# Performance work log

Hardware: AMD Instinct MI355X
Metric: run time of the kernel (lower is better)

The kernel has to match this reference:

```python
import jax, jax.numpy as jnp
import numpy as np

D = 1024   # visual_dim
N = 64     # num_phrases(1) * topN(64)
DEG = 16   # edges per subject row (incl. one guaranteed via a permutation)
E = N * DEG
T = 2      # cfg.MODEL.RELATION.VISUAL_GRAPH_PASSING_TIME


def _graph():
    rng = np.random.default_rng(0)
    perm = rng.permutation(N)
    mask = np.zeros((N, N), bool)
    for i in range(N):
        mask[i, perm[i]] = True  # permutation guarantees every column is covered
        pool = np.delete(np.arange(N), perm[i])
        mask[i, rng.choice(pool, DEG - 1, replace=False)] = True
    hdim, wdim = np.nonzero(mask)  # row-major, exactly E entries
    conn = np.full((N, N), -1, np.int32)
    conn[hdim, wdim] = np.arange(hdim.shape[0])
    edge_idx = hdim * N + wdim  # original: hdim*topN + wdim (topN == N since num_phrases == 1)
    return conn, edge_idx.astype(np.int32)


def setup_inputs():
    conn, edge_idx = _graph()
    key = jax.random.key(0)
    ks = jax.random.split(key, 16)
    p = lambda k, shp: jax.random.normal(k, shp, jnp.float32) * 0.02
    return {
        'visual_feat': jax.random.normal(ks[0], (N, D), jnp.float32),
        'rel_visual_feat': jax.random.normal(ks[1], (E, D), jnp.float32),
        'conn_map': jnp.asarray(conn),
        'topN_boxes_ids': jnp.arange(N, dtype=jnp.int32)[None, :],  # only shape is used
        'edge_idx': jnp.asarray(edge_idx),
        'W_sub': p(ks[2], (D, D)),
        'W_obj': p(ks[3], (D, D)),
        'W_r2s': p(ks[4], (D, D)),
        'W_r2o': p(ks[5], (D, D)),
        'W_joint': p(ks[6], (D, 4 * D)),
        'W_ctx': p(ks[7], (D, 3 * D)),
        'W_rel_update': p(ks[8], (D, 3 * D)),
        'W_rel_joint': p(ks[9], (D, 4 * D)),
        'W_rel_ctx': p(ks[10], (D, 2 * D)),
        'W_node': p(ks[11], (D, 2 * D)),
        'b_node': jnp.zeros((D,), jnp.float32),
        'W_factor': p(ks[12], (D, 2 * D)),
    }


def _forward(visual_feat, rel_visual_feat, conn_map, edge_idx,
             W_sub, W_obj, W_r2s, W_r2o, W_joint, W_ctx, W_rel_update,
             W_rel_joint, W_rel_ctx, W_node, b_node, W_factor):
    n, d = visual_feat.shape
    scale = jnp.asarray(d, visual_feat.dtype) ** 0.5
    connected = conn_map >= 0
    # scatter edge features into the dense [N, N, D] grid
    rel_temp = (jnp.zeros((n * n, d), visual_feat.dtype)
                .at[edge_idx].set(rel_visual_feat)
                .reshape(n, n, d))
    rel_ctx = rel_temp
    vctx = visual_feat
    for _ in range(T):
        # joint node embedding  [N, D]
        vj = jnp.concatenate([visual_feat, vctx, visual_feat * vctx, vctx - visual_feat], 1) @ W_joint.T
        # joint edge embedding  [N, N, D] (1x1 conv == per-position linear)
        rj = jnp.einsum('ijd,od->ijo',
                        jnp.concatenate([rel_temp, rel_ctx, rel_temp * rel_ctx, rel_temp - rel_ctx], 2),
                        W_rel_joint)
        # node -> edge: cat(sub_tile, obj_tile, rj) @ W_rel_update, done without tiling
        Ws, Wo, Wr = W_rel_update[:, :d], W_rel_update[:, d:2 * d], W_rel_update[:, 2 * d:]
        rel_j = (vj @ Ws.T)[:, None, :] + (vj @ Wo.T)[None, :, :] + jnp.einsum('ijd,od->ijo', rj, Wr)
        # edge -> node attention scores (elementwise product of 1x1-conv outputs, summed over channels)
        s_sbj = jnp.einsum('id,ijd->ij', vj @ W_sub.T, jnp.einsum('ijd,od->ijo', rel_j, W_r2s)) / scale
        s_obj = jnp.einsum('jd,ijd->ij', vj @ W_obj.T, jnp.einsum('ijd,od->ijo', rel_j, W_r2o)) / scale
        w_sbj = jax.nn.softmax(jnp.where(connected, s_sbj, -jnp.inf), axis=1)
        w_obj = jax.nn.softmax(jnp.where(connected, s_obj, -jnp.inf), axis=0)
        ctx = jnp.concatenate([jnp.einsum('ijd,ij->id', rel_j, w_sbj),
                               jnp.einsum('ijd,ij->jd', rel_j, w_obj)], 1)
        vctx = jnp.concatenate([vctx, ctx], 1) @ W_ctx.T
        rel_ctx = jnp.einsum('ijd,od->ijo', jnp.concatenate([rel_ctx, rel_j], 2), W_rel_ctx)
    # gather back the valid edges and produce outputs
    rel_out = jnp.concatenate([rel_visual_feat, rel_ctx.reshape(-1, d)[edge_idx]], 1) @ W_factor.T
    v_out = jnp.concatenate([visual_feat, vctx], 1) @ W_node.T + b_node
    deg = connected.sum(1) + connected.sum(0)
    v_out = jnp.where((deg == 0)[:, None], visual_feat, v_out)  # isolated nodes pass through
    return rel_out, v_out


def reference(visual_feat, rel_visual_feat, conn_map, topN_boxes_ids, edge_idx,
              W_sub, W_obj, W_r2s, W_r2o, W_joint, W_ctx, W_rel_update,
              W_rel_joint, W_rel_ctx, W_node, b_node, W_factor):
    del topN_boxes_ids  # only its shape is used in the original
    return _forward(visual_feat, rel_visual_feat, conn_map, edge_idx,
                    W_sub, W_obj, W_r2s, W_r2o, W_joint, W_ctx, W_rel_update,
                    W_rel_joint, W_rel_ctx, W_node, b_node, W_factor)
```

## Files before the change

kernel.cpp:

```cpp
#include <hip/hip_runtime.h>

static constexpr int kN = 64;
static constexpr int kD = 1024;
static constexpr int kE = 1024;
static constexpr int kT = 2;

typedef short  bf16x8 __attribute__((ext_vector_type(8)));
typedef float  f32x4  __attribute__((ext_vector_type(4)));
typedef unsigned short us8 __attribute__((ext_vector_type(8)));
typedef unsigned short us4 __attribute__((ext_vector_type(4)));

__device__ __forceinline__ unsigned short f2b(float f) {
    unsigned int u = __builtin_bit_cast(unsigned int, f);
    u += 0x7FFFu + ((u >> 16) & 1u);
    return (unsigned short)(u >> 16);
}
__device__ __forceinline__ float b2f(unsigned short u) {
    unsigned int x = ((unsigned int)u) << 16;
    return __builtin_bit_cast(float, x);
}
__device__ __forceinline__ bf16x8 cvt8(float4 a, float4 b) {
    us8 o;
    o[0] = f2b(a.x); o[1] = f2b(a.y); o[2] = f2b(a.z); o[3] = f2b(a.w);
    o[4] = f2b(b.x); o[5] = f2b(b.y); o[6] = f2b(b.z); o[7] = f2b(b.w);
    return __builtin_bit_cast(bf16x8, o);
}

struct ASrc { const unsigned short* s0; const unsigned short* s1; const unsigned short* s2;
              int mode; int ld; };

__device__ __forceinline__ bf16x8 loadA8(const ASrc& s, int row, int kg) {
    const int seg = kg >> 10, k = kg & 1023;
    const size_t ro = (size_t)row * s.ld + k;
    if (s.mode == 1) {
        const unsigned short* p = (seg == 0) ? s.s0 : (seg == 1 ? s.s1 : s.s2);
        return *(const bf16x8*)(p + ro);
    }
    const bf16x8 a = *(const bf16x8*)(s.s0 + ro);
    if (seg == 0) return a;
    const bf16x8 b = *(const bf16x8*)(s.s1 + ro);
    const us8 ua = __builtin_bit_cast(us8, a), ub = __builtin_bit_cast(us8, b);
    us8 o;
#pragma unroll
    for (int q = 0; q < 8; ++q) o[q] = f2b(b2f(ua[q]) * b2f(ub[q]));
    return __builtin_bit_cast(bf16x8, o);
}

struct GJob { ASrc a; const unsigned short* W; int ldw; void* P; int M; int K; int KS; int pbf; };
struct GJobs { GJob j[8]; int t0[9]; int nj; };

__global__ __launch_bounds__(256)
void k_gemm(GJobs G)
{
    __shared__ unsigned short lds[12288];
    const int flat = blockIdx.x;
    int ji = 0;
    while (ji + 1 < G.nj && flat >= G.t0[ji + 1]) ++ji;
    const GJob J = G.j[ji];
    const int local = flat - G.t0[ji];
    const int rowTiles = J.M >> 6;
    const int rt = local & (rowTiles - 1);
    const int rest = local / rowTiles;
    const int ct = rest & 7, z = rest >> 3;
    const int rowBase = rt * 64, colBase = ct * 128;
    const int kchunk = J.K / J.KS, kbeg = z * kchunk, kend = kbeg + kchunk;

    const int tid = threadIdx.x, lane = tid & 63, wid = tid >> 6;
    const int l15 = lane & 15, l4 = lane >> 4;
    const int sr = tid >> 3, sc8 = tid & 7;
    const int wc8 = (sc8 ^ (sr & 7)) * 8;
    const int wr = wid >> 1, wc = wid & 1;

    bf16x8 ra[2], rb[4];
    auto stage = [&](int kt) {
#pragma unroll
        for (int h = 0; h < 2; ++h)
            ra[h] = loadA8(J.a, rowBase + sr + 32 * h, kt + sc8 * 8);
#pragma unroll
        for (int h = 0; h < 4; ++h)
            rb[h] = *(const bf16x8*)(J.W + (size_t)(colBase + sr + 32 * h) * J.ldw + kt + sc8 * 8);
    };

    f32x4 acc[2][4] = {};
    stage(kbeg);
    for (int kt = kbeg; kt < kend; kt += 64) {
        __syncthreads();
#pragma unroll
        for (int h = 0; h < 2; ++h)
            *(bf16x8*)&lds[(sr + 32 * h) * 64 + wc8] = ra[h];
#pragma unroll
        for (int h = 0; h < 4; ++h)
            *(bf16x8*)&lds[4096 + (sr + 32 * h) * 64 + wc8] = rb[h];
        __syncthreads();
        if (kt + 64 < kend) stage(kt + 64);
#pragma unroll
        for (int kk = 0; kk < 2; ++kk) {
            const int c8 = kk * 4 + l4;
            bf16x8 af[2], bv[4];
#pragma unroll
            for (int m = 0; m < 2; ++m) {
                const int ar = wr * 32 + m * 16 + l15;
                af[m] = *(const bf16x8*)&lds[ar * 64 + (c8 ^ (ar & 7)) * 8];
            }
#pragma unroll
            for (int n = 0; n < 4; ++n) {
                const int br = wc * 64 + n * 16 + l15;
                bv[n] = *(const bf16x8*)&lds[4096 + br * 64 + (c8 ^ (br & 7)) * 8];
            }
#pragma unroll
            for (int m = 0; m < 2; ++m)
#pragma unroll
                for (int n = 0; n < 4; ++n)
                    acc[m][n] = __builtin_amdgcn_mfma_f32_16x16x32_bf16(af[m], bv[n], acc[m][n], 0, 0, 0);
        }
    }

    if (J.pbf) {
        __syncthreads();
#pragma unroll
        for (int m = 0; m < 2; ++m)
#pragma unroll
            for (int n = 0; n < 4; ++n)
#pragma unroll
                for (int r = 0; r < 4; ++r)
                    lds[(wr * 32 + m * 16 + l4 * 4 + r) * 132 + wc * 64 + n * 16 + l15] =
                        f2b(acc[m][n][r]);
        __syncthreads();
        unsigned short* Pb = (unsigned short*)J.P + (size_t)z * J.M * 1024;
#pragma unroll
        for (int c = tid; c < 1024; c += 256) {
            const int row = c >> 4, ch = c & 15;
            *(bf16x8*)(Pb + (size_t)(rowBase + row) * 1024 + colBase + ch * 8) =
                *(const bf16x8*)&lds[row * 132 + ch * 8];
        }
    } else {
        float* base = (float*)J.P + (size_t)z * J.M * 1024;
#pragma unroll
        for (int m = 0; m < 2; ++m) {
            const int row = rowBase + wr * 32 + m * 16 + l4 * 4;
#pragma unroll
            for (int n = 0; n < 4; ++n) {
                const int col = colBase + wc * 64 + n * 16 + l15;
#pragma unroll
                for (int r = 0; r < 4; ++r)
                    base[(size_t)(row + r) * 1024 + col] = acc[m][n][r];
            }
        }
    }
}

struct RJob { const void* P; int MO8; int KS; int pbf; float* Cf; unsigned short* Cb;
              const unsigned short* addb; const float* bias; int gather;
              const float* gP; int ostride; };
struct RJobs { RJob j[8]; int t0[9]; int nj; const int* eidx; int gKS; };

__global__ void k_reduce(RJobs R)
{
    const int flat = blockIdx.x;
    int ji = 0;
    while (ji + 1 < R.nj && flat >= R.t0[ji + 1]) ++ji;
    const RJob J = R.j[ji];
    const int i8 = (flat - R.t0[ji]) * 256 + threadIdx.x;
    if (i8 >= J.MO8) return;
    float s[8] = {0.f, 0.f, 0.f, 0.f, 0.f, 0.f, 0.f, 0.f};
    if (J.pbf) {
        const unsigned short* P = (const unsigned short*)J.P;
        for (int z = 0; z < J.KS; ++z) {
            const us8 v = *(const us8*)(P + (size_t)z * J.MO8 * 8 + (size_t)i8 * 8);
#pragma unroll
            for (int q = 0; q < 8; ++q) s[q] += b2f(v[q]);
        }
    } else {
        const float* P = (const float*)J.P;
        for (int z = 0; z < J.KS; ++z) {
            const float* p = P + (size_t)z * J.MO8 * 8 + (size_t)i8 * 8;
            const float4 v0 = *(const float4*)p;
            const float4 v1 = *(const float4*)(p + 4);
            s[0] += v0.x; s[1] += v0.y; s[2] += v0.z; s[3] += v0.w;
            s[4] += v1.x; s[5] += v1.y; s[6] += v1.z; s[7] += v1.w;
        }
    }
    if (J.addb) {
        const us8 v = *(const us8*)(J.addb + (size_t)i8 * 8);
#pragma unroll
        for (int q = 0; q < 8; ++q) s[q] += b2f(v[q]);
    }
    if (J.gather) {
        const int e = i8 >> 7, c8 = i8 & 127;
        const int idx = R.eidx[e];
        const float* as_ = J.gP + (size_t)(idx >> 6) * 1024 + c8 * 8;
        const float* ao_ = J.gP + 131072 + (size_t)(idx & 63) * 1024 + c8 * 8;
        for (int z = 0; z < R.gKS; ++z) {
#pragma unroll
            for (int q = 0; q < 8; ++q)
                s[q] += as_[(size_t)z * 65536 + q] + ao_[(size_t)z * 65536 + q];
        }
    }
    if (J.bias) {
        const int c8 = i8 & 127;
#pragma unroll
        for (int q = 0; q < 8; ++q) s[q] += J.bias[c8 * 8 + q];
    }
    if (J.Cf) {
        *(float4*)(J.Cf + (size_t)i8 * 8)     = make_float4(s[0], s[1], s[2], s[3]);
        *(float4*)(J.Cf + (size_t)i8 * 8 + 4) = make_float4(s[4], s[5], s[6], s[7]);
    }
    if (J.Cb) {
        us8 o;
#pragma unroll
        for (int q = 0; q < 8; ++q) o[q] = f2b(s[q]);
        if (J.ostride) {
            const int row = i8 >> 7, c8 = i8 & 127;
            *(us8*)(J.Cb + (size_t)row * J.ostride + c8 * 8) = o;
        } else {
            *(us8*)(J.Cb + (size_t)i8 * 8) = o;
        }
    }
}

struct ConvBatch { const float* s[7]; unsigned short* d[7]; int beg8[7]; int total8; };
__global__ void k_f2b_batch(ConvBatch cb)
{
    int i = blockIdx.x * blockDim.x + threadIdx.x;
    if (i >= cb.total8) return;
    int k = 0;
    while (k < 6 && i >= cb.beg8[k + 1]) ++k;
    const int j = i - cb.beg8[k];
    const float4 v0 = reinterpret_cast<const float4*>(cb.s[k])[2 * j];
    const float4 v1 = reinterpret_cast<const float4*>(cb.s[k])[2 * j + 1];
    const bf16x8 o = cvt8(v0, v1);
    *(bf16x8*)(cb.d[k] + (size_t)j * 8) = o;
}

struct TJ { const float* s; unsigned short* d; int ld; };
struct T7 { TJ t[7]; };
__global__ __launch_bounds__(256)
void k_transpose(T7 t7)
{
    __shared__ float tile[64][65];
    const TJ tj = t7.t[blockIdx.z];
    const int bx = blockIdx.x * 64, by = blockIdx.y * 64;
    const int c = threadIdx.x & 63, r0 = threadIdx.x >> 6;
#pragma unroll
    for (int h = 0; h < 16; ++h) {
        const int r = r0 * 16 + h;
        tile[r][c] = tj.s[(size_t)(by + r) * tj.ld + bx + c];
    }
    __syncthreads();
#pragma unroll
    for (int h = 0; h < 16; ++h) {
        const int kk = r0 * 16 + h;
        tj.d[(size_t)(bx + kk) * 1024 + by + c] = f2b(tile[c][kk]);
    }
}

__global__ __launch_bounds__(256)
void k_buildW(const float* __restrict__ Wrel, const float* __restrict__ Wjnt,
              unsigned short* __restrict__ WrtRel, unsigned short* __restrict__ WeffRel,
              unsigned short* __restrict__ UrtVj, unsigned short* __restrict__ UeffVj)
{
    const int idx = blockIdx.x * 256 + threadIdx.x;
    const int o = idx >> 8, j = (idx & 255) * 4;
    const float* W = blockIdx.z ? Wjnt : Wrel;
    const float sgn = blockIdx.z ? -1.f : 1.f;
    unsigned short* rt = blockIdx.z ? UrtVj : WrtRel;
    unsigned short* ef = blockIdx.z ? UeffVj : WeffRel;
    const float4 w1 = *(const float4*)(W + (size_t)o * 4096 + j);
    const float4 w2 = *(const float4*)(W + (size_t)o * 4096 + 1024 + j);
    const float4 w3 = *(const float4*)(W + (size_t)o * 4096 + 2048 + j);
    const float4 w4 = *(const float4*)(W + (size_t)o * 4096 + 3072 + j);
    us4 t;
    t.x = f2b(w1.x + sgn * w4.x); t.y = f2b(w1.y + sgn * w4.y);
    t.z = f2b(w1.z + sgn * w4.z); t.w = f2b(w1.w + sgn * w4.w);
    *(us4*)(rt + (size_t)o * 1024 + j) = t;
    t.x = f2b(w2.x - sgn * w4.x); t.y = f2b(w2.y - sgn * w4.y);
    t.z = f2b(w2.z - sgn * w4.z); t.w = f2b(w2.w - sgn * w4.w);
    *(us4*)(ef + (size_t)o * 2048 + j) = t;
    t.x = f2b(w3.x); t.y = f2b(w3.y); t.z = f2b(w3.z); t.w = f2b(w3.w);
    *(us4*)(ef + (size_t)o * 2048 + 1024 + j) = t;
}

__global__ __launch_bounds__(256)
void k_sctx(const float* __restrict__ relj, const float* __restrict__ qws,
            const float* __restrict__ qwo, const int* __restrict__ conn,
            unsigned short* __restrict__ ctx1b, unsigned short* __restrict__ ctx2b)
{
    const int bid = blockIdx.x, t = threadIdx.x;
    const float4* relj4 = reinterpret_cast<const float4*>(relj);
    __shared__ float sl[64];
    __shared__ int el[64];
    float4 acc = make_float4(0.f, 0.f, 0.f, 0.f);

    if (bid < 64) {
        const int i = bid;
        {
            const int g = t >> 4, l = t & 15;
            const size_t e4 = (size_t)(i * 16 + g) * 256;
            const float4* q4 = reinterpret_cast<const float4*>(qws) + (size_t)i * 256;
            float v = 0.f;
#pragma unroll
            for (int q = 0; q < 16; ++q) {
                const float4 r = relj4[e4 + l + q * 16];
                const float4 a = q4[l + q * 16];
                v += a.x * r.x + a.y * r.y + a.z * r.z + a.w * r.w;
            }
            v += __shfl_xor(v, 1, 16);
            v += __shfl_xor(v, 2, 16);
            v += __shfl_xor(v, 4, 16);
            v += __shfl_xor(v, 8, 16);
            if (l == 0) sl[g] = v * 0.03125f;
        }
        __syncthreads();
        float sv[16];
        float m = -1e30f;
#pragma unroll
        for (int q = 0; q < 16; ++q) { sv[q] = sl[q]; m = fmaxf(m, sv[q]); }
        float sum = 0.f;
#pragma unroll
        for (int q = 0; q < 16; ++q) { sv[q] = expf(sv[q] - m); sum += sv[q]; }
        const float inv = 1.f / sum;
#pragma unroll
        for (int q = 0; q < 16; ++q) {
            const float w = sv[q] * inv;
            const float4 v = relj4[(size_t)(i * 16 + q) * 256 + t];
            acc.x += w * v.x; acc.y += w * v.y; acc.z += w * v.z; acc.w += w * v.w;
        }
        us4 o; o.x = f2b(acc.x); o.y = f2b(acc.y); o.z = f2b(acc.z); o.w = f2b(acc.w);
        *(us4*)(ctx1b + (size_t)i * 1024 + t * 4) = o;
    } else {
        const int j = bid - 64;
        {
            const int i = t >> 2, sub = t & 3;
            const int e = conn[i * kN + j];
            if (sub == 0) el[i] = e;
            float v = 0.f;
            if (e >= 0) {
                const size_t e4 = (size_t)e * 256;
                const float4* q4 = reinterpret_cast<const float4*>(qwo) + (size_t)j * 256;
#pragma unroll
                for (int q = 0; q < 64; ++q) {
                    const float4 r = relj4[e4 + sub + q * 4];
                    const float4 a = q4[sub + q * 4];
                    v += a.x * r.x + a.y * r.y + a.z * r.z + a.w * r.w;
                }
            }
            v += __shfl_xor(v, 1, 4);
            v += __shfl_xor(v, 2, 4);
            if (sub == 0) sl[i] = (e >= 0) ? v * 0.03125f : -1e30f;
        }
        __syncthreads();
        float m = -1e30f;
        for (int i = 0; i < 64; ++i) m = fmaxf(m, sl[i]);
        float sum = 0.f;
        float ex[64];
        for (int i = 0; i < 64; ++i) {
            ex[i] = (el[i] >= 0) ? expf(sl[i] - m) : 0.f;
            sum += ex[i];
        }
        const float inv = 1.f / sum;
        for (int i = 0; i < 64; ++i) {
            const int e = el[i];
            if (e >= 0) {
                const float w = ex[i] * inv;
                const float4 v = relj4[(size_t)e * 256 + t];
                acc.x += w * v.x; acc.y += w * v.y; acc.z += w * v.z; acc.w += w * v.w;
            }
        }
        us4 o; o.x = f2b(acc.x); o.y = f2b(acc.y); o.z = f2b(acc.z); o.w = f2b(acc.w);
        *(us4*)(ctx2b + (size_t)j * 1024 + t * 4) = o;
    }
}

extern "C" void kernel_launch(void* const* d_in, const int* in_sizes, int n_in,
                              void* d_out, int out_size, void* d_ws, size_t ws_size,
                              hipStream_t stream)
{
    const float* visual   = (const float*)d_in[0];
    const float* relvis   = (const float*)d_in[1];
    const int*   conn     = (const int*)d_in[2];
    const int*   edge_idx = (const int*)d_in[4];
    const float* W_sub    = (const float*)d_in[5];
    const float* W_obj    = (const float*)d_in[6];
    const float* W_r2s    = (const float*)d_in[7];
    const float* W_r2o    = (const float*)d_in[8];
    const float* W_joint  = (const float*)d_in[9];
    const float* W_ctx    = (const float*)d_in[10];
    const float* W_relu   = (const float*)d_in[11];
    const float* W_relj   = (const float*)d_in[12];
    const float* W_relc   = (const float*)d_in[13];
    const float* W_node   = (const float*)d_in[14];
    const float* b_node   = (const float*)d_in[15];
    const float* W_factor = (const float*)d_in[16];
    (void)in_sizes; (void)n_in; (void)out_size; (void)ws_size;

    float* ws = (float*)d_ws;
    size_t off = 0;
    auto allocF = [&](size_t n) { float* p = ws + off; off += n; return p; };
    auto allocU = [&](size_t n) { return (unsigned short*)allocF((n + 1) / 2); };

    float* partF = allocF((size_t)1024 * 1024);
    unsigned short* partB = allocU((size_t)16 * 1024 * 1024);
    float* asqw  = allocF((size_t)4 * 64 * 1024);
    float* relj  = allocF((size_t)kE * kD);
    unsigned short* relvis_b = allocU((size_t)kE * kD);
    unsigned short* visual_b = allocU((size_t)kN * kD);
    unsigned short* vj_b   = allocU((size_t)kN * kD);
    unsigned short* rj_b   = allocU((size_t)kE * kD);
    unsigned short* rc_bA  = allocU((size_t)kE * kD);
    unsigned short* rc_bB  = allocU((size_t)kE * kD);
    unsigned short* vctx_bA = allocU((size_t)kN * kD);
    unsigned short* vctx_bB = allocU((size_t)kN * kD);
    unsigned short* ctx1_b = allocU((size_t)kN * kD);
    unsigned short* ctx2_b = allocU((size_t)kN * kD);
    unsigned short* R0_b = allocU((size_t)kE * kD);
    unsigned short* G0_b = allocU((size_t)kN * kD);
    unsigned short* Wb_ctx    = allocU((size_t)kD * 3 * kD);
    unsigned short* Wb_relu   = allocU((size_t)kD * 3 * kD);
    unsigned short* Wb_relc   = allocU((size_t)kD * 2 * kD);
    unsigned short* Wb_node   = allocU((size_t)kD * 2 * kD);
    unsigned short* Wb_factor = allocU((size_t)kD * 2 * kD);
    unsigned short* WsubT = allocU((size_t)kD * kD);
    unsigned short* WobjT = allocU((size_t)kD * kD);
    unsigned short* Wr2sT = allocU((size_t)kD * kD);
    unsigned short* Wr2oT = allocU((size_t)kD * kD);
    unsigned short* WsT   = allocU((size_t)kD * kD);
    unsigned short* WoT   = allocU((size_t)kD * kD);
    unsigned short* WrT   = allocU((size_t)kD * kD);
    unsigned short* Wc_s  = allocU((size_t)kD * kD);
    unsigned short* Wc_o  = allocU((size_t)kD * kD);
    unsigned short* Wso2  = allocU((size_t)kD * kD);
    unsigned short* Woo2  = allocU((size_t)kD * kD);
    unsigned short* WrtRel  = allocU((size_t)kD * kD);
    unsigned short* WeffRel = allocU((size_t)kD * 2 * kD);
    unsigned short* UrtVj   = allocU((size_t)kD * kD);
    unsigned short* UeffVj  = allocU((size_t)kD * 2 * kD);

    auto seg1 = [](const unsigned short* a, int ld = 1024) {
        ASrc s; s.s0 = a; s.s1 = nullptr; s.s2 = nullptr; s.mode = 1; s.ld = ld; return s;
    };
    auto seg2 = [](const unsigned short* a, const unsigned short* b) {
        ASrc s; s.s0 = a; s.s1 = b; s.s2 = nullptr; s.mode = 1; s.ld = 1024; return s;
    };
    auto seg3 = [](const unsigned short* a, const unsigned short* b, const unsigned short* c) {
        ASrc s; s.s0 = a; s.s1 = b; s.s2 = c; s.mode = 1; s.ld = 1024; return s;
    };
    auto prodA = [](const unsigned short* c, const unsigned short* x) {
        ASrc s; s.s0 = c; s.s1 = x; s.s2 = nullptr; s.mode = 2; s.ld = 1024; return s;
    };

    GJobs G; RJobs R;
    int gn = 0, gt = 0, rn = 0, rtt = 0;
    auto gAdd = [&](ASrc a, const unsigned short* W, int ldw, void* P, int M, int K, int KS, int pbf) {
        G.j[gn].a = a; G.j[gn].W = W; G.j[gn].ldw = ldw; G.j[gn].P = P;
        G.j[gn].M = M; G.j[gn].K = K; G.j[gn].KS = KS; G.j[gn].pbf = pbf;
        G.t0[gn] = gt; gt += KS * (M >> 6) * 8; ++gn;
    };
    auto gLaunch = [&]() {
        G.nj = gn; G.t0[gn] = gt;
        hipLaunchKernelGGL(k_gemm, dim3(gt), dim3(256), 0, stream, G);
        gn = 0; gt = 0;
    };
    auto rAdd = [&](const void* P, int MO8, int KS, int pbf, float* Cf, unsigned short* Cb,
                    const unsigned short* addb, const float* bias,
                    const float* gP, int ostride) {
        R.j[rn].P = P; R.j[rn].MO8 = MO8; R.j[rn].KS = KS; R.j[rn].pbf = pbf;
        R.j[rn].Cf = Cf; R.j[rn].Cb = Cb; R.j[rn].addb = addb; R.j[rn].bias = bias;
        R.j[rn].gather = (gP != nullptr); R.j[rn].gP = gP; R.j[rn].ostride = ostride;
        R.t0[rn] = rtt; rtt += (MO8 + 255) / 256; ++rn;
    };
    auto rLaunch = [&](const int* eidx, int gKS) {
        R.nj = rn; R.t0[rn] = rtt; R.eidx = eidx; R.gKS = gKS;
        hipLaunchKernelGGL(k_reduce, dim3(rtt), dim3(256), 0, stream, R);
        rn = 0; rtt = 0;
    };

    {
        ConvBatch cb;
        const float* srcs[7] = {W_ctx, W_relu, W_relc, W_node, W_factor, relvis, visual};
        unsigned short* dsts[7] = {Wb_ctx, Wb_relu, Wb_relc, Wb_node, Wb_factor, relvis_b, visual_b};
        const int nel[7] = {3 * 1024 * 1024, 3 * 1024 * 1024, 2 * 1024 * 1024,
                            2 * 1024 * 1024, 2 * 1024 * 1024, 1024 * 1024, 64 * 1024};
        int cum = 0;
        for (int k = 0; k < 7; ++k) { cb.s[k] = srcs[k]; cb.d[k] = dsts[k]; cb.beg8[k] = cum; cum += nel[k] / 8; }
        cb.total8 = cum;
        hipLaunchKernelGGL(k_f2b_batch, dim3((cum + 255) / 256), dim3(256), 0, stream, cb);
    }
    {
        T7 t7;
        t7.t[0] = {W_sub, WsubT, 1024};
        t7.t[1] = {W_obj, WobjT, 1024};
        t7.t[2] = {W_r2s, Wr2sT, 1024};
        t7.t[3] = {W_r2o, Wr2oT, 1024};
        t7.t[4] = {W_relu,        WsT, 3072};
        t7.t[5] = {W_relu + 1024, WoT, 3072};
        t7.t[6] = {W_relu + 2048, WrT, 3072};
        hipLaunchKernelGGL(k_transpose, dim3(16, 16, 7), dim3(256), 0, stream, t7);
    }
    hipLaunchKernelGGL(k_buildW, dim3(1024, 1, 2), dim3(256), 0, stream,
                       W_relj, W_joint, WrtRel, WeffRel, UrtVj, UeffVj);

    const size_t PB2 = (size_t)2 * 1024 * 1024;
    gAdd(seg1(Wr2sT), WsubT, 1024, partB,           1024, 1024, 2, 1);
    gAdd(seg1(Wr2oT), WobjT, 1024, partB + PB2,     1024, 1024, 2, 1);
    gAdd(seg1(relvis_b), WrtRel, 1024, partB + 2 * PB2, 1024, 1024, 2, 1);
    gAdd(seg1(Wb_relc + 1024, 2048), WrT, 1024, partB + 3 * PB2, 1024, 1024, 2, 1);
    gAdd(seg1(Wb_relc + 1024, 2048), WsT, 1024, partB + 4 * PB2, 1024, 1024, 2, 1);
    gAdd(seg1(Wb_relc + 1024, 2048), WoT, 1024, partB + 5 * PB2, 1024, 1024, 2, 1);
    gAdd(seg1(visual_b), UrtVj, 1024, partF, 64, 1024, 4, 0);
    gLaunch();
    rAdd(partB,           131072, 2, 1, nullptr, Wc_s, nullptr, nullptr, nullptr, 0);
    rAdd(partB + PB2,     131072, 2, 1, nullptr, Wc_o, nullptr, nullptr, nullptr, 0);
    rAdd(partB + 2 * PB2, 131072, 2, 1, nullptr, R0_b, nullptr, nullptr, nullptr, 0);
    rAdd(partB + 3 * PB2, 131072, 2, 1, nullptr, Wb_relc + 1024, nullptr, nullptr, nullptr, 2048);
    rAdd(partB + 4 * PB2, 131072, 2, 1, nullptr, Wso2, nullptr, nullptr, nullptr, 0);
    rAdd(partB + 5 * PB2, 131072, 2, 1, nullptr, Woo2, nullptr, nullptr, nullptr, 0);
    rAdd(partF, 8192, 4, 0, nullptr, G0_b, nullptr, nullptr, nullptr, 0);
    rLaunch(nullptr, 0);

    for (int t = 0; t < kT; ++t) {
        const unsigned short* vcur  = (t == 0) ? visual_b : vctx_bA;
        unsigned short*       vnext = (t == 0) ? vctx_bA : vctx_bB;
        const unsigned short* rccur = (t == 0) ? relvis_b : rc_bA;
        unsigned short*       rcnext = (t == 0) ? rc_bA : rc_bB;

        gAdd(prodA(vcur, visual_b), UeffVj, 2048, partF, 64, 2048, 8, 0);
        gAdd(prodA(rccur, relvis_b), WeffRel, 2048, partB, 1024, 2048, 8, 1);
        gLaunch();
        rAdd(partF, 8192, 8, 0, nullptr, vj_b, G0_b, nullptr, nullptr, 0);
        rAdd(partB, 131072, 8, 1, nullptr, rj_b, R0_b, nullptr, nullptr, 0);
        rLaunch(nullptr, 0);

        gAdd(seg1(vj_b), Wb_relu,        3072, partF,          64, 1024, 2, 0);
        gAdd(seg1(vj_b), Wb_relu + 1024, 3072, partF + 131072, 64, 1024, 2, 0);
        gAdd(seg1(vj_b), Wc_s,           1024, partF + 262144, 64, 1024, 2, 0);
        gAdd(seg1(vj_b), Wc_o,           1024, partF + 393216, 64, 1024, 2, 0);
        gAdd(seg1(vj_b), Wso2,           1024, partF + 524288, 64, 1024, 2, 0);
        gAdd(seg1(vj_b), Woo2,           1024, partF + 655360, 64, 1024, 2, 0);
        gAdd(seg1(rj_b), Wb_relu + 2048, 3072, partB,        1024, 1024, 4, 1);
        gAdd(seg2(rccur, rj_b), Wb_relc, 2048, partB + 8388608, 1024, 2048, 8, 1);
        gLaunch();
        rAdd(partF + 262144, 8192, 2, 0, asqw + 131072, nullptr, nullptr, nullptr, nullptr, 0);
        rAdd(partF + 393216, 8192, 2, 0, asqw + 196608, nullptr, nullptr, nullptr, nullptr, 0);
        rAdd(partB, 131072, 4, 1, relj, nullptr, nullptr, nullptr, partF, 0);
        rAdd(partB + 8388608, 131072, 8, 1, nullptr, rcnext, nullptr, nullptr, partF + 524288, 0);
        rLaunch(edge_idx, 2);

        hipLaunchKernelGGL(k_sctx, dim3(128), dim3(256), 0, stream,
                           relj, asqw + 131072, asqw + 196608, conn, ctx1_b, ctx2_b);

        gAdd(seg3(vcur, ctx1_b, ctx2_b), Wb_ctx, 3072, partF, 64, 3072, 8, 0);
        gLaunch();
        rAdd(partF, 8192, 8, 0, nullptr, vnext, nullptr, nullptr, nullptr, 0);
        rLaunch(nullptr, 0);
    }

    float* rel_out = (float*)d_out;
    float* v_out   = (float*)d_out + (size_t)kE * kD;
    gAdd(seg2(relvis_b, rc_bB), Wb_factor, 2048, partB, 1024, 2048, 4, 1);
    gAdd(seg2(visual_b, vctx_bB), Wb_node, 2048, partF, 64, 2048, 8, 0);
    gLaunch();
    rAdd(partB, 131072, 4, 1, rel_out, nullptr, nullptr, nullptr, nullptr, 0);
    rAdd(partF, 8192, 8, 0, v_out, nullptr, nullptr, b_node, nullptr, 0);
    rLaunch(nullptr, 0);
}
```

Baseline: 233.3 us.

## Fold relation-joint weights into downstream update and context weights

```diff
diff --git a/kernel.cpp b/kernel.cpp
--- a/kernel.cpp
+++ b/kernel.cpp
@@ -150,7 +150,7 @@
 }
 
 struct RJob { const void* P; int MO8; int KS; int pbf; float* Cf; unsigned short* Cb;
-              const unsigned short* addb; const float* bias; int gather;
+              const unsigned short* addb; int astride; const float* bias; int gather;
               const float* gP; int ostride; };
 struct RJobs { RJob j[8]; int t0[9]; int nj; const int* eidx; int gKS; };
 
@@ -181,7 +181,9 @@
         }
     }
     if (J.addb) {
-        const us8 v = *(const us8*)(J.addb + (size_t)i8 * 8);
+        const us8 v = J.astride
+            ? *(const us8*)(J.addb + (size_t)(i8 >> 7) * J.astride + (i8 & 127) * 8)
+            : *(const us8*)(J.addb + (size_t)i8 * 8);
 #pragma unroll
         for (int q = 0; q < 8; ++q) s[q] += b2f(v[q]);
     }
@@ -232,19 +234,23 @@
     *(bf16x8*)(cb.d[k] + (size_t)j * 8) = o;
 }
 
-struct TJ { const float* s; unsigned short* d; int ld; };
-struct T7 { TJ t[7]; };
+struct TJ { const void* s; unsigned short* d; int ld; int cols; int isbf; };
+struct T8 { TJ t[8]; };
 __global__ __launch_bounds__(256)
-void k_transpose(T7 t7)
-{
+void k_transpose(T8 t8)
+{
+    const TJ tj = t8.t[blockIdx.z];
+    const int bx = blockIdx.x * 64, by = blockIdx.y * 64;
+    if (bx >= tj.cols) return;
     __shared__ float tile[64][65];
-    const TJ tj = t7.t[blockIdx.z];
-    const int bx = blockIdx.x * 64, by = blockIdx.y * 64;
     const int c = threadIdx.x & 63, r0 = threadIdx.x >> 6;
 #pragma unroll
     for (int h = 0; h < 16; ++h) {
         const int r = r0 * 16 + h;
-        tile[r][c] = tj.s[(size_t)(by + r) * tj.ld + bx + c];
+        float v;
+        if (tj.isbf) v = b2f(((const unsigned short*)tj.s)[(size_t)(by + r) * tj.ld + bx + c]);
+        else         v = ((const float*)tj.s)[(size_t)(by + r) * tj.ld + bx + c];
+        tile[r][c] = v;
     }
     __syncthreads();
 #pragma unroll
@@ -405,15 +411,16 @@
     unsigned short* relvis_b = allocU((size_t)kE * kD);
     unsigned short* visual_b = allocU((size_t)kN * kD);
     unsigned short* vj_b   = allocU((size_t)kN * kD);
-    unsigned short* rj_b   = allocU((size_t)kE * kD);
     unsigned short* rc_bA  = allocU((size_t)kE * kD);
     unsigned short* rc_bB  = allocU((size_t)kE * kD);
     unsigned short* vctx_bA = allocU((size_t)kN * kD);
     unsigned short* vctx_bB = allocU((size_t)kN * kD);
     unsigned short* ctx1_b = allocU((size_t)kN * kD);
     unsigned short* ctx2_b = allocU((size_t)kN * kD);
-    unsigned short* R0_b = allocU((size_t)kE * kD);
-    unsigned short* G0_b = allocU((size_t)kN * kD);
+    unsigned short* R0_b  = allocU((size_t)kE * kD);
+    unsigned short* R0r_b = allocU((size_t)kE * kD);
+    unsigned short* R0c_b = allocU((size_t)kE * kD);
+    unsigned short* G0_b  = allocU((size_t)kN * kD);
     unsigned short* Wb_ctx    = allocU((size_t)kD * 3 * kD);
     unsigned short* Wb_relu   = allocU((size_t)kD * 3 * kD);
     unsigned short* Wb_relc   = allocU((size_t)kD * 2 * kD);
@@ -432,6 +439,9 @@
     unsigned short* Woo2  = allocU((size_t)kD * kD);
     unsigned short* WrtRel  = allocU((size_t)kD * kD);
     unsigned short* WeffRel = allocU((size_t)kD * 2 * kD);
+    unsigned short* WeffT   = allocU((size_t)2 * kD * kD);
+    unsigned short* Weffr   = allocU((size_t)kD * 2 * kD);
+    unsigned short* Wcomb   = allocU((size_t)kD * 2 * kD);
     unsigned short* UrtVj   = allocU((size_t)kD * kD);
     unsigned short* UeffVj  = allocU((size_t)kD * 2 * kD);
 
@@ -461,11 +471,12 @@
         gn = 0; gt = 0;
     };
     auto rAdd = [&](const void* P, int MO8, int KS, int pbf, float* Cf, unsigned short* Cb,
-                    const unsigned short* addb, const float* bias,
+                    const unsigned short* addb, int astride, const float* bias,
                     const float* gP, int ostride) {
         R.j[rn].P = P; R.j[rn].MO8 = MO8; R.j[rn].KS = KS; R.j[rn].pbf = pbf;
-        R.j[rn].Cf = Cf; R.j[rn].Cb = Cb; R.j[rn].addb = addb; R.j[rn].bias = bias;
-        R.j[rn].gather = (gP != nullptr); R.j[rn].gP = gP; R.j[rn].ostride = ostride;
+        R.j[rn].Cf = Cf; R.j[rn].Cb = Cb; R.j[rn].addb = addb; R.j[rn].astride = astride;
+        R.j[rn].bias = bias; R.j[rn].gather = (gP != nullptr); R.j[rn].gP = gP;
+        R.j[rn].ostride = ostride;
         R.t0[rn] = rtt; rtt += (MO8 + 255) / 256; ++rn;
     };
     auto rLaunch = [&](const int* eidx, int gKS) {
@@ -485,19 +496,20 @@
         cb.total8 = cum;
         hipLaunchKernelGGL(k_f2b_batch, dim3((cum + 255) / 256), dim3(256), 0, stream, cb);
     }
-    {
-        T7 t7;
-        t7.t[0] = {W_sub, WsubT, 1024};
-        t7.t[1] = {W_obj, WobjT, 1024};
-        t7.t[2] = {W_r2s, Wr2sT, 1024};
-        t7.t[3] = {W_r2o, Wr2oT, 1024};
-        t7.t[4] = {W_relu,        WsT, 3072};
-        t7.t[5] = {W_relu + 1024, WoT, 3072};
-        t7.t[6] = {W_relu + 2048, WrT, 3072};
-        hipLaunchKernelGGL(k_transpose, dim3(16, 16, 7), dim3(256), 0, stream, t7);
-    }
     hipLaunchKernelGGL(k_buildW, dim3(1024, 1, 2), dim3(256), 0, stream,
                        W_relj, W_joint, WrtRel, WeffRel, UrtVj, UeffVj);
+    {
+        T8 t8;
+        t8.t[0] = {W_sub, WsubT, 1024, 1024, 0};
+        t8.t[1] = {W_obj, WobjT, 1024, 1024, 0};
+        t8.t[2] = {W_r2s, Wr2sT, 1024, 1024, 0};
+        t8.t[3] = {W_r2o, Wr2oT, 1024, 1024, 0};
+        t8.t[4] = {W_relu,        WsT, 3072, 1024, 0};
+        t8.t[5] = {W_relu + 1024, WoT, 3072, 1024, 0};
+        t8.t[6] = {W_relu + 2048, WrT, 3072, 1024, 0};
+        t8.t[7] = {WeffRel, WeffT, 2048, 2048, 1};
+        hipLaunchKernelGGL(k_transpose, dim3(32, 16, 8), dim3(256), 0, stream, t8);
+    }
 
     const size_t PB2 = (size_t)2 * 1024 * 1024;
     gAdd(seg1(Wr2sT), WsubT, 1024, partB,           1024, 1024, 2, 1);
@@ -508,13 +520,28 @@
     gAdd(seg1(Wb_relc + 1024, 2048), WoT, 1024, partB + 5 * PB2, 1024, 1024, 2, 1);
     gAdd(seg1(visual_b), UrtVj, 1024, partF, 64, 1024, 4, 0);
     gLaunch();
-    rAdd(partB,           131072, 2, 1, nullptr, Wc_s, nullptr, nullptr, nullptr, 0);
-    rAdd(partB + PB2,     131072, 2, 1, nullptr, Wc_o, nullptr, nullptr, nullptr, 0);
-    rAdd(partB + 2 * PB2, 131072, 2, 1, nullptr, R0_b, nullptr, nullptr, nullptr, 0);
-    rAdd(partB + 3 * PB2, 131072, 2, 1, nullptr, Wb_relc + 1024, nullptr, nullptr, nullptr, 2048);
-    rAdd(partB + 4 * PB2, 131072, 2, 1, nullptr, Wso2, nullptr, nullptr, nullptr, 0);
-    rAdd(partB + 5 * PB2, 131072, 2, 1, nullptr, Woo2, nullptr, nullptr, nullptr, 0);
-    rAdd(partF, 8192, 4, 0, nullptr, G0_b, nullptr, nullptr, nullptr, 0);
+    rAdd(partB,           131072, 2, 1, nullptr, Wc_s, nullptr, 0, nullptr, nullptr, 0);
+    rAdd(partB + PB2,     131072, 2, 1, nullptr, Wc_o, nullptr, 0, nullptr, nullptr, 0);
+    rAdd(partB + 2 * PB2, 131072, 2, 1, nullptr, R0_b, nullptr, 0, nullptr, nullptr, 0);
+    rAdd(partB + 3 * PB2, 131072, 2, 1, nullptr, Wb_relc + 1024, nullptr, 0, nullptr, nullptr, 2048);
+    rAdd(partB + 4 * PB2, 131072, 2, 1, nullptr, Wso2, nullptr, 0, nullptr, nullptr, 0);
+    rAdd(partB + 5 * PB2, 131072, 2, 1, nullptr, Woo2, nullptr, 0, nullptr, nullptr, 0);
+    rAdd(partF, 8192, 4, 0, nullptr, G0_b, nullptr, 0, nullptr, nullptr, 0);
+    rLaunch(nullptr, 0);
+
+    gAdd(seg1(Wb_relu + 2048, 3072), WeffT,                 1024, partB,           1024, 1024, 2, 1);
+    gAdd(seg1(Wb_relu + 2048, 3072), WeffT + 1024 * 1024,   1024, partB + PB2,     1024, 1024, 2, 1);
+    gAdd(seg1(Wb_relc + 1024, 2048), WeffT,                 1024, partB + 2 * PB2, 1024, 1024, 2, 1);
+    gAdd(seg1(Wb_relc + 1024, 2048), WeffT + 1024 * 1024,   1024, partB + 3 * PB2, 1024, 1024, 2, 1);
+    gAdd(seg1(R0_b), Wb_relu + 2048, 3072, partB + 4 * PB2, 1024, 1024, 2, 1);
+    gAdd(seg1(R0_b), Wb_relc + 1024, 2048, partB + 5 * PB2, 1024, 1024, 2, 1);
+    gLaunch();
+    rAdd(partB,           131072, 2, 1, nullptr, Weffr,        nullptr, 0,    nullptr, nullptr, 2048);
+    rAdd(partB + PB2,     131072, 2, 1, nullptr, Weffr + 1024, nullptr, 0,    nullptr, nullptr, 2048);
+    rAdd(partB + 2 * PB2, 131072, 2, 1, nullptr, Wcomb,        Wb_relc, 2048, nullptr, nullptr, 2048);
+    rAdd(partB + 3 * PB2, 131072, 2, 1, nullptr, Wcomb + 1024, nullptr, 0,    nullptr, nullptr, 2048);
+    rAdd(partB + 4 * PB2, 131072, 2, 1, nullptr, R0r_b, nullptr, 0, nullptr, nullptr, 0);
+    rAdd(partB + 5 * PB2, 131072, 2, 1, nullptr, R0c_b, nullptr, 0, nullptr, nullptr, 0);
     rLaunch(nullptr, 0);
 
     for (int t = 0; t < kT; ++t) {
@@ -524,10 +551,10 @@
         unsigned short*       rcnext = (t == 0) ? rc_bA : rc_bB;
 
         gAdd(prodA(vcur, visual_b), UeffVj, 2048, partF, 64, 2048, 8, 0);
-        gAdd(prodA(rccur, relvis_b), WeffRel, 2048, partB, 1024, 2048, 8, 1);
+        gAdd(prodA(rccur, relvis_b), Weffr, 2048, partB,                 1024, 2048, 4, 1);
+        gAdd(prodA(rccur, relvis_b), Wcomb, 2048, partB + 4 * 1024 * 1024, 1024, 2048, 4, 1);
         gLaunch();
-        rAdd(partF, 8192, 8, 0, nullptr, vj_b, G0_b, nullptr, nullptr, 0);
-        rAdd(partB, 131072, 8, 1, nullptr, rj_b, R0_b, nullptr, nullptr, 0);
+        rAdd(partF, 8192, 8, 0, nullptr, vj_b, G0_b, 0, nullptr, nullptr, 0);
         rLaunch(nullptr, 0);
 
         gAdd(seg1(vj_b), Wb_relu,        3072, partF,          64, 1024, 2, 0);
@@ -536,13 +563,11 @@
         gAdd(seg1(vj_b), Wc_o,           1024, partF + 393216, 64, 1024, 2, 0);
         gAdd(seg1(vj_b), Wso2,           1024, partF + 524288, 64, 1024, 2, 0);
         gAdd(seg1(vj_b), Woo2,           1024, partF + 655360, 64, 1024, 2, 0);
-        gAdd(seg1(rj_b), Wb_relu + 2048, 3072, partB,        1024, 1024, 4, 1);
-        gAdd(seg2(rccur, rj_b), Wb_relc, 2048, partB + 8388608, 1024, 2048, 8, 1);
         gLaunch();
-        rAdd(partF + 262144, 8192, 2, 0, asqw + 131072, nullptr, nullptr, nullptr, nullptr, 0);
-        rAdd(partF + 393216, 8192, 2, 0, asqw + 196608, nullptr, nullptr, nullptr, nullptr, 0);
-        rAdd(partB, 131072, 4, 1, relj, nullptr, nullptr, nullptr, partF, 0);
-        rAdd(partB + 8388608, 131072, 8, 1, nullptr, rcnext, nullptr, nullptr, partF + 524288, 0);
+        rAdd(partF + 262144, 8192, 2, 0, asqw + 131072, nullptr, nullptr, 0, nullptr, nullptr, 0);
+        rAdd(partF + 393216, 8192, 2, 0, asqw + 196608, nullptr, nullptr, 0, nullptr, nullptr, 0);
+        rAdd(partB, 131072, 4, 1, relj, nullptr, R0r_b, 0, nullptr, partF, 0);
+        rAdd(partB + 4 * 1024 * 1024, 131072, 4, 1, nullptr, rcnext, R0c_b, 0, nullptr, partF + 524288, 0);
         rLaunch(edge_idx, 2);
 
         hipLaunchKernelGGL(k_sctx, dim3(128), dim3(256), 0, stream,
@@ -550,7 +575,7 @@
 
         gAdd(seg3(vcur, ctx1_b, ctx2_b), Wb_ctx, 3072, partF, 64, 3072, 8, 0);
         gLaunch();
-        rAdd(partF, 8192, 8, 0, nullptr, vnext, nullptr, nullptr, nullptr, 0);
+        rAdd(partF, 8192, 8, 0, nullptr, vnext, nullptr, 0, nullptr, nullptr, 0);
         rLaunch(nullptr, 0);
     }
 
@@ -559,7 +584,7 @@
     gAdd(seg2(relvis_b, rc_bB), Wb_factor, 2048, partB, 1024, 2048, 4, 1);
     gAdd(seg2(visual_b, vctx_bB), Wb_node, 2048, partF, 64, 2048, 8, 0);
     gLaunch();
-    rAdd(partB, 131072, 4, 1, rel_out, nullptr, nullptr, nullptr, nullptr, 0);
-    rAdd(partF, 8192, 8, 0, v_out, nullptr, nullptr, b_node, nullptr, 0);
+    rAdd(partB, 131072, 4, 1, rel_out, nullptr, nullptr, 0, nullptr, nullptr, 0);
+    rAdd(partF, 8192, 8, 0, v_out, nullptr, nullptr, 0, b_node, nullptr, 0);
     rLaunch(nullptr, 0);
 }
```

Result: slower. 275.5 us (+18.1%).
